# Optimization experiments

Measured on AMD Instinct MI355X. Metric: run time of the kernel, lower is better.

Reference implementation:

```python
import jax, jax.numpy as jnp
import numpy as np

B, L, H = 4, 96, 512
R, T = 257, 21


def setup_inputs() -> dict:
    key = jax.random.key(0)
    ks = jax.random.split(key, 7)
    std_in = (2.0 / (H + 1 + R)) ** 0.5  # xavier_normal over [H+1, R]
    return {
        "layer1": jax.random.normal(ks[0], (B, L, H), jnp.float32),
        "layer2": jax.random.normal(ks[1], (B, L, H), jnp.float32),
        "layer3": jax.random.normal(ks[2], (B, L, H), jnp.float32),
        "W_1": jax.random.normal(ks[3], (H + 1, R), jnp.float32) * std_in,
        "W_2": jax.random.normal(ks[4], (H + 1, R), jnp.float32) * std_in,
        "W_3": jax.random.normal(ks[5], (H + 1, R), jnp.float32) * std_in,
        "W_l": jax.random.normal(ks[6], (1, R, T), jnp.float32),
    }


def reference(layer1, layer2, layer3, W_1, W_2, W_3, W_l):
    # Append bias-ones feature, as in the torch forward.
    ones = jnp.ones((*layer1.shape[:2], 1), layer1.dtype)
    l1 = jnp.concatenate([layer1, ones], axis=-1)  # [n, i, H+1]
    l2 = jnp.concatenate([layer2, ones], axis=-1)  # [n, j, H+1]
    l3 = jnp.concatenate([layer3, jnp.ones((*layer3.shape[:-1], 1), layer3.dtype)], axis=-1)
    # Factor the CP contraction: project each stream to rank space first.
    p1 = jnp.einsum("nia,ar->nir", l1, W_1)  # [n, i, r]
    p2 = jnp.einsum("njb,br->njr", l2, W_2)  # [n, j, r]
    p3 = jnp.einsum("nkc,cr->nkr", l3, W_3)  # [n, k, r]
    # Fold label map into one stream, then rank-reduce outer product.
    p3t = jnp.einsum("nkr,rt->ntkr", p3, W_l[0])  # [n, t, k, r]
    out = jnp.einsum("nir,njr,ntkr->ntijk", p1, p2, p3t)  # [n, t, i, j, k]
    return out
```

## Files before the change

### kernel.cpp

```cpp
#include <hip/hip_runtime.h>
#include <hip/hip_bf16.h>

#define RR 257
#define RP 288
#define TT 21

typedef __attribute__((ext_vector_type(4))) float f32x4;
typedef __attribute__((ext_vector_type(8))) short bf16x8;

union Pack8 { unsigned short s[8]; uint4 v; };

__device__ __forceinline__ unsigned short f2b(float f) {
    union { float f; unsigned u; } v; v.f = f;
    unsigned r = v.u + 0x7fffu + ((v.u >> 16) & 1u);
    return (unsigned short)(r >> 16);
}

__global__ __launch_bounds__(384) void proj_kernel(
    const float* __restrict__ l1, const float* __restrict__ l2, const float* __restrict__ l3,
    const float* __restrict__ W1, const float* __restrict__ W2, const float* __restrict__ W3,
    float* __restrict__ P1f, float* __restrict__ P2f, float* __restrict__ P3f)
{
    int bx = blockIdx.x;
    int grp = bx % 24;
    int n = (bx / 24) & 3;
    int s = bx / 96;
    const float* layer = (s == 0) ? l1 : (s == 1) ? l2 : l3;
    const float* W     = (s == 0) ? W1 : (s == 1) ? W2 : W3;
    int i0 = grp * 4;

    __shared__ __attribute__((aligned(16))) float x[2048];
    const float4* src = (const float4*)(layer + (n * 96 + i0) * 512);
    float4* xv = (float4*)x;
    for (int idx = threadIdx.x; idx < 512; idx += 384) xv[idx] = src[idx];
    __syncthreads();

    int r = threadIdx.x;
    if (r < RP) {
        float a0 = 0.f, a1 = 0.f, a2 = 0.f, a3 = 0.f;
        if (r < RR) {
            float b = W[512 * RR + r];
            a0 = a1 = a2 = a3 = b;
            #pragma unroll 8
            for (int a = 0; a < 512; ++a) {
                float wa = W[a * RR + r];
                a0 = fmaf(x[a], wa, a0);
                a1 = fmaf(x[512 + a], wa, a1);
                a2 = fmaf(x[1024 + a], wa, a2);
                a3 = fmaf(x[1536 + a], wa, a3);
            }
        }
        float* P = (s == 0) ? P1f : (s == 1) ? P2f : P3f;
        int base = (n * 96 + i0) * RP + r;
        P[base]          = a0;
        P[base + RP]     = a1;
        P[base + 2 * RP] = a2;
        P[base + 3 * RP] = a3;
    }
}

__global__ __launch_bounds__(256) void aprep_kernel(
    const float* __restrict__ P1f, const float* __restrict__ P2f,
    unsigned short* __restrict__ Af)
{
    int bx = blockIdx.x;
    int n = bx / 96, i = bx % 96;
    __shared__ __attribute__((aligned(16))) float p1row[RP];
    for (int r = threadIdx.x; r < RP; r += 256)
        p1row[r] = P1f[(n * 96 + i) * RP + r];
    __syncthreads();

    unsigned short* dst = Af + (size_t)(n * 576 + i * 6) * 9 * 512;
    for (int idx = threadIdx.x; idx < 3456; idx += 256) {
        int L = idx & 63;
        int rest = idx >> 6;
        int ks = rest % 9, rgl = rest / 9;
        int j = rgl * 16 + (L & 15);
        int k8 = ks * 32 + (L >> 4) * 8;
        const float* p2p = P2f + (n * 96 + j) * RP + k8;
        float4 b0 = *(const float4*)(p2p);
        float4 b1 = *(const float4*)(p2p + 4);
        float4 a0 = *(const float4*)(p1row + k8);
        float4 a1 = *(const float4*)(p1row + k8 + 4);
        Pack8 u;
        u.s[0] = f2b(a0.x * b0.x); u.s[1] = f2b(a0.y * b0.y);
        u.s[2] = f2b(a0.z * b0.z); u.s[3] = f2b(a0.w * b0.w);
        u.s[4] = f2b(a1.x * b1.x); u.s[5] = f2b(a1.y * b1.y);
        u.s[6] = f2b(a1.z * b1.z); u.s[7] = f2b(a1.w * b1.w);
        *(uint4*)(dst + (size_t)(rgl * 9 + ks) * 512 + L * 8) = u.v;
    }
}

__global__ __launch_bounds__(256) void bprep_kernel(
    const float* __restrict__ P3f, const float* __restrict__ Wl,
    unsigned short* __restrict__ Bf)
{
    int bx = blockIdx.x;
    int t = bx % TT, n = bx / TT;
    __shared__ __attribute__((aligned(16))) float wl_lds[RP];
    for (int r = threadIdx.x; r < RP; r += 256)
        wl_lds[r] = (r < RR) ? Wl[r * TT + t] : 0.f;
    __syncthreads();

    unsigned short* dst = Bf + (size_t)(n * TT + t) * 6 * 9 * 512;
    for (int idx = threadIdx.x; idx < 3456; idx += 256) {
        int L = idx & 63;
        int rest = idx >> 6;
        int ks = rest % 9, kg = rest / 9;
        int col = kg * 16 + (L & 15);
        int r8 = ks * 32 + (L >> 4) * 8;
        const float* p3p = P3f + (n * 96 + col) * RP + r8;
        float4 p0 = *(const float4*)(p3p);
        float4 p1 = *(const float4*)(p3p + 4);
        float4 w0 = *(const float4*)(wl_lds + r8);
        float4 w1 = *(const float4*)(wl_lds + r8 + 4);
        Pack8 u;
        u.s[0] = f2b(p0.x * w0.x); u.s[1] = f2b(p0.y * w0.y);
        u.s[2] = f2b(p0.z * w0.z); u.s[3] = f2b(p0.w * w0.w);
        u.s[4] = f2b(p1.x * w1.x); u.s[5] = f2b(p1.y * w1.y);
        u.s[6] = f2b(p1.z * w1.z); u.s[7] = f2b(p1.w * w1.w);
        *(uint4*)(dst + (size_t)(kg * 9 + ks) * 512 + L * 8) = u.v;
    }
}

#define LOADA(s, kss) { _Pragma("unroll") for (int mf = 0; mf < 4; ++mf) \
    fa[s][mf] = *(const bf16x8*)(abase + (mf * 9 + (kss)) * 512); }
#define LOADB(s, kss) { _Pragma("unroll") for (int nf = 0; nf < 6; ++nf) \
    fb[s][nf] = *(const bf16x8*)(bbase + (nf * 9 + (kss)) * 512); }
#define MFMAS(s) { _Pragma("unroll") for (int mf = 0; mf < 4; ++mf) { \
    _Pragma("unroll") for (int nf = 0; nf < 6; ++nf) \
      acc[mf][nf] = __builtin_amdgcn_mfma_f32_16x16x32_bf16(fb[s][nf], fa[s][mf], acc[mf][nf], 0, 0, 0); } }

__global__ __launch_bounds__(256, 2) void tri4_kernel(
    const unsigned short* __restrict__ Af, const unsigned short* __restrict__ Bf,
    float* __restrict__ out)
{
    int orig = blockIdx.x;
    int bx = (orig & 7) * 378 + (orig >> 3);
    int t = bx % TT;
    int mtn = bx / TT;
    int mt = mtn % 36;
    int n = mtn / 36;

    int tid = threadIdx.x, lane = tid & 63, wv = tid >> 6;

    const unsigned short* abase = Af + (size_t)(n * 576 + mt * 16 + wv * 4) * 9 * 512 + lane * 8;
    const unsigned short* bbase = Bf + (size_t)(n * TT + t) * 6 * 9 * 512 + lane * 8;

    f32x4 acc[4][6] = {};
    bf16x8 fa[2][4], fb[2][6];

    LOADA(0, 0); LOADB(0, 0);
    #pragma unroll
    for (int kp = 0; kp < 4; ++kp) {
        LOADA(1, 2 * kp + 1); LOADB(1, 2 * kp + 1);
        MFMAS(0);
        LOADA(0, 2 * kp + 2); LOADB(0, 2 * kp + 2);
        MFMAS(1);
    }
    MFMAS(0);

    __shared__ __attribute__((aligned(16))) float tbuf[4][1600];
    int Llo = lane & 15, Lhi = lane >> 4;
    size_t outbase = ((size_t)(n * TT + t) * 9216 + mt * 256 + wv * 64) * 96;

    #pragma unroll
    for (int mf = 0; mf < 4; ++mf) {
        #pragma unroll
        for (int nf = 0; nf < 6; ++nf)
            *(f32x4*)&tbuf[wv][Llo * 100 + nf * 16 + Lhi * 4] = acc[mf][nf];
        float* gdst = out + outbase + (size_t)mf * 16 * 96;
        #pragma unroll
        for (int q = 0; q < 6; ++q) {
            int fidx = q * 64 + lane;
            int ml = fidx / 24, k4 = fidx % 24;
            f32x4 vv = *(const f32x4*)&tbuf[wv][ml * 100 + k4 * 4];
            __builtin_nontemporal_store(vv, (f32x4*)(gdst + (size_t)fidx * 4));
        }
    }
}

extern "C" void kernel_launch(void* const* d_in, const int* in_sizes, int n_in,
                              void* d_out, int out_size, void* d_ws, size_t ws_size,
                              hipStream_t stream) {
    const float* l1 = (const float*)d_in[0];
    const float* l2 = (const float*)d_in[1];
    const float* l3 = (const float*)d_in[2];
    const float* W1 = (const float*)d_in[3];
    const float* W2 = (const float*)d_in[4];
    const float* W3 = (const float*)d_in[5];
    const float* Wl = (const float*)d_in[6];

    float* P1f = (float*)d_ws;
    float* P2f = P1f + 384 * RP;
    float* P3f = P2f + 384 * RP;
    unsigned short* Af = (unsigned short*)(P3f + 384 * RP);
    unsigned short* Bf = Af + (size_t)4 * 576 * 9 * 512;

    proj_kernel<<<288, 384, 0, stream>>>(l1, l2, l3, W1, W2, W3, P1f, P2f, P3f);
    aprep_kernel<<<384, 256, 0, stream>>>(P1f, P2f, Af);
    bprep_kernel<<<84, 256, 0, stream>>>(P3f, Wl, Bf);
    tri4_kernel<<<3024, 256, 0, stream>>>(Af, Bf, (float*)d_out);
}
```

Before: 116.6 us.

## Split projection finer, fuse A/B prep kernels, use single-wave output blocks with staggered start

The projection kernel now computes two rows per block instead of four, doubling the grid. The A-prep and B-prep kernels are merged into one launch, with B work split in half across block pairs. The main MFMA kernel drops from four waves per block to one wave per block, quadrupling the grid to 12096 blocks. The first 2048 blocks sleep for a small pseudo-random delay to stagger their write traffic. These changes aim to cut launch count and tail effects, at the risk of more scheduling overhead and idle sleep time.

```diff
diff --git a/kernel.cpp b/kernel.cpp
--- a/kernel.cpp
+++ b/kernel.cpp
@@ -22,104 +22,100 @@
     float* __restrict__ P1f, float* __restrict__ P2f, float* __restrict__ P3f)
 {
     int bx = blockIdx.x;
-    int grp = bx % 24;
-    int n = (bx / 24) & 3;
-    int s = bx / 96;
+    int grp = bx % 48;
+    int n = (bx / 48) & 3;
+    int s = bx / 192;
     const float* layer = (s == 0) ? l1 : (s == 1) ? l2 : l3;
     const float* W     = (s == 0) ? W1 : (s == 1) ? W2 : W3;
-    int i0 = grp * 4;
-
-    __shared__ __attribute__((aligned(16))) float x[2048];
+    int i0 = grp * 2;
+
+    __shared__ __attribute__((aligned(16))) float x[1024];
     const float4* src = (const float4*)(layer + (n * 96 + i0) * 512);
     float4* xv = (float4*)x;
-    for (int idx = threadIdx.x; idx < 512; idx += 384) xv[idx] = src[idx];
+    for (int idx = threadIdx.x; idx < 256; idx += 384) xv[idx] = src[idx];
     __syncthreads();
 
     int r = threadIdx.x;
     if (r < RP) {
-        float a0 = 0.f, a1 = 0.f, a2 = 0.f, a3 = 0.f;
+        float a0 = 0.f, a1 = 0.f;
         if (r < RR) {
             float b = W[512 * RR + r];
-            a0 = a1 = a2 = a3 = b;
+            a0 = a1 = b;
             #pragma unroll 8
             for (int a = 0; a < 512; ++a) {
                 float wa = W[a * RR + r];
                 a0 = fmaf(x[a], wa, a0);
                 a1 = fmaf(x[512 + a], wa, a1);
-                a2 = fmaf(x[1024 + a], wa, a2);
-                a3 = fmaf(x[1536 + a], wa, a3);
             }
         }
         float* P = (s == 0) ? P1f : (s == 1) ? P2f : P3f;
         int base = (n * 96 + i0) * RP + r;
-        P[base]          = a0;
-        P[base + RP]     = a1;
-        P[base + 2 * RP] = a2;
-        P[base + 3 * RP] = a3;
-    }
-}
-
-__global__ __launch_bounds__(256) void aprep_kernel(
+        P[base]      = a0;
+        P[base + RP] = a1;
+    }
+}
+
+__global__ __launch_bounds__(256) void prep_kernel(
     const float* __restrict__ P1f, const float* __restrict__ P2f,
-    unsigned short* __restrict__ Af)
+    const float* __restrict__ P3f, const float* __restrict__ Wl,
+    unsigned short* __restrict__ Af, unsigned short* __restrict__ Bf)
 {
     int bx = blockIdx.x;
-    int n = bx / 96, i = bx % 96;
-    __shared__ __attribute__((aligned(16))) float p1row[RP];
-    for (int r = threadIdx.x; r < RP; r += 256)
-        p1row[r] = P1f[(n * 96 + i) * RP + r];
-    __syncthreads();
-
-    unsigned short* dst = Af + (size_t)(n * 576 + i * 6) * 9 * 512;
-    for (int idx = threadIdx.x; idx < 3456; idx += 256) {
-        int L = idx & 63;
-        int rest = idx >> 6;
-        int ks = rest % 9, rgl = rest / 9;
-        int j = rgl * 16 + (L & 15);
-        int k8 = ks * 32 + (L >> 4) * 8;
-        const float* p2p = P2f + (n * 96 + j) * RP + k8;
-        float4 b0 = *(const float4*)(p2p);
-        float4 b1 = *(const float4*)(p2p + 4);
-        float4 a0 = *(const float4*)(p1row + k8);
-        float4 a1 = *(const float4*)(p1row + k8 + 4);
-        Pack8 u;
-        u.s[0] = f2b(a0.x * b0.x); u.s[1] = f2b(a0.y * b0.y);
-        u.s[2] = f2b(a0.z * b0.z); u.s[3] = f2b(a0.w * b0.w);
-        u.s[4] = f2b(a1.x * b1.x); u.s[5] = f2b(a1.y * b1.y);
-        u.s[6] = f2b(a1.z * b1.z); u.s[7] = f2b(a1.w * b1.w);
-        *(uint4*)(dst + (size_t)(rgl * 9 + ks) * 512 + L * 8) = u.v;
-    }
-}
-
-__global__ __launch_bounds__(256) void bprep_kernel(
-    const float* __restrict__ P3f, const float* __restrict__ Wl,
-    unsigned short* __restrict__ Bf)
-{
-    int bx = blockIdx.x;
-    int t = bx % TT, n = bx / TT;
-    __shared__ __attribute__((aligned(16))) float wl_lds[RP];
-    for (int r = threadIdx.x; r < RP; r += 256)
-        wl_lds[r] = (r < RR) ? Wl[r * TT + t] : 0.f;
-    __syncthreads();
-
-    unsigned short* dst = Bf + (size_t)(n * TT + t) * 6 * 9 * 512;
-    for (int idx = threadIdx.x; idx < 3456; idx += 256) {
-        int L = idx & 63;
-        int rest = idx >> 6;
-        int ks = rest % 9, kg = rest / 9;
-        int col = kg * 16 + (L & 15);
-        int r8 = ks * 32 + (L >> 4) * 8;
-        const float* p3p = P3f + (n * 96 + col) * RP + r8;
-        float4 p0 = *(const float4*)(p3p);
-        float4 p1 = *(const float4*)(p3p + 4);
-        float4 w0 = *(const float4*)(wl_lds + r8);
-        float4 w1 = *(const float4*)(wl_lds + r8 + 4);
-        Pack8 u;
-        u.s[0] = f2b(p0.x * w0.x); u.s[1] = f2b(p0.y * w0.y);
-        u.s[2] = f2b(p0.z * w0.z); u.s[3] = f2b(p0.w * w0.w);
-        u.s[4] = f2b(p1.x * w1.x); u.s[5] = f2b(p1.y * w1.y);
-        u.s[6] = f2b(p1.z * w1.z); u.s[7] = f2b(p1.w * w1.w);
-        *(uint4*)(dst + (size_t)(kg * 9 + ks) * 512 + L * 8) = u.v;
+    if (bx < 384) {
+        int n = bx / 96, i = bx % 96;
+        __shared__ __attribute__((aligned(16))) float p1row[RP];
+        for (int r = threadIdx.x; r < RP; r += 256)
+            p1row[r] = P1f[(n * 96 + i) * RP + r];
+        __syncthreads();
+
+        unsigned short* dst = Af + (size_t)(n * 576 + i * 6) * 9 * 512;
+        for (int idx = threadIdx.x; idx < 3456; idx += 256) {
+            int L = idx & 63;
+            int rest = idx >> 6;
+            int ks = rest % 9, rgl = rest / 9;
+            int j = rgl * 16 + (L & 15);
+            int k8 = ks * 32 + (L >> 4) * 8;
+            const float* p2p = P2f + (n * 96 + j) * RP + k8;
+            float4 b0 = *(const float4*)(p2p);
+            float4 b1 = *(const float4*)(p2p + 4);
+            float4 a0 = *(const float4*)(p1row + k8);
+            float4 a1 = *(const float4*)(p1row + k8 + 4);
+            Pack8 u;
+            u.s[0] = f2b(a0.x * b0.x); u.s[1] = f2b(a0.y * b0.y);
+            u.s[2] = f2b(a0.z * b0.z); u.s[3] = f2b(a0.w * b0.w);
+            u.s[4] = f2b(a1.x * b1.x); u.s[5] = f2b(a1.y * b1.y);
+            u.s[6] = f2b(a1.z * b1.z); u.s[7] = f2b(a1.w * b1.w);
+            *(uint4*)(dst + (size_t)(rgl * 9 + ks) * 512 + L * 8) = u.v;
+        }
+    } else {
+        int b2 = bx - 384;
+        int h = b2 & 1;
+        int t = (b2 >> 1) % TT, n = b2 / (2 * TT);
+        __shared__ __attribute__((aligned(16))) float wl_lds[RP];
+        for (int r = threadIdx.x; r < RP; r += 256)
+            wl_lds[r] = (r < RR) ? Wl[r * TT + t] : 0.f;
+        __syncthreads();
+
+        unsigned short* dst = Bf + (size_t)(n * TT + t) * 6 * 9 * 512;
+        for (int idx2 = threadIdx.x; idx2 < 1728; idx2 += 256) {
+            int idx = h * 1728 + idx2;
+            int L = idx & 63;
+            int rest = idx >> 6;
+            int ks = rest % 9, kg = rest / 9;
+            int col = kg * 16 + (L & 15);
+            int r8 = ks * 32 + (L >> 4) * 8;
+            const float* p3p = P3f + (n * 96 + col) * RP + r8;
+            float4 p0 = *(const float4*)(p3p);
+            float4 p1 = *(const float4*)(p3p + 4);
+            float4 w0 = *(const float4*)(wl_lds + r8);
+            float4 w1 = *(const float4*)(wl_lds + r8 + 4);
+            Pack8 u;
+            u.s[0] = f2b(p0.x * w0.x); u.s[1] = f2b(p0.y * w0.y);
+            u.s[2] = f2b(p0.z * w0.z); u.s[3] = f2b(p0.w * w0.w);
+            u.s[4] = f2b(p1.x * w1.x); u.s[5] = f2b(p1.y * w1.y);
+            u.s[6] = f2b(p1.z * w1.z); u.s[7] = f2b(p1.w * w1.w);
+            *(uint4*)(dst + (size_t)(kg * 9 + ks) * 512 + L * 8) = u.v;
+        }
     }
 }
 
@@ -131,21 +127,27 @@
     _Pragma("unroll") for (int nf = 0; nf < 6; ++nf) \
       acc[mf][nf] = __builtin_amdgcn_mfma_f32_16x16x32_bf16(fb[s][nf], fa[s][mf], acc[mf][nf], 0, 0, 0); } }
 
-__global__ __launch_bounds__(256, 2) void tri4_kernel(
+__global__ __launch_bounds__(64, 2) void tri12_kernel(
     const unsigned short* __restrict__ Af, const unsigned short* __restrict__ Bf,
     float* __restrict__ out)
 {
     int orig = blockIdx.x;
-    int bx = (orig & 7) * 378 + (orig >> 3);
+    if (orig < 2048) {
+        int key = ((orig >> 3) ^ (orig >> 8)) & 7;
+        for (int d = 0; d < key; ++d) __builtin_amdgcn_s_sleep(16);
+    }
+    int bx = (orig & 7) * 1512 + (orig >> 3);
     int t = bx % TT;
     int mtn = bx / TT;
-    int mt = mtn % 36;
-    int n = mtn / 36;
-
-    int tid = threadIdx.x, lane = tid & 63, wv = tid >> 6;
-
-    const unsigned short* abase = Af + (size_t)(n * 576 + mt * 16 + wv * 4) * 9 * 512 + lane * 8;
-    const unsigned short* bbase = Bf + (size_t)(n * TT + t) * 6 * 9 * 512 + lane * 8;
+    int mt = mtn % 144;
+    int n = mtn / 144;
+
+    int lane = threadIdx.x & 63;
+
+    const unsigned short* abase =
+        Af + (size_t)(n * 576 + mt * 4) * 9 * 512 + lane * 8;
+    const unsigned short* bbase =
+        Bf + (size_t)(n * TT + t) * 27648 + lane * 8;
 
     f32x4 acc[4][6] = {};
     bf16x8 fa[2][4], fb[2][6];
@@ -160,21 +162,21 @@
     }
     MFMAS(0);
 
-    __shared__ __attribute__((aligned(16))) float tbuf[4][1600];
+    __shared__ __attribute__((aligned(16))) float tb[1600];
     int Llo = lane & 15, Lhi = lane >> 4;
-    size_t outbase = ((size_t)(n * TT + t) * 9216 + mt * 256 + wv * 64) * 96;
+    size_t outbase = ((size_t)(n * TT + t) * 9216 + mt * 64) * 96;
 
     #pragma unroll
     for (int mf = 0; mf < 4; ++mf) {
         #pragma unroll
         for (int nf = 0; nf < 6; ++nf)
-            *(f32x4*)&tbuf[wv][Llo * 100 + nf * 16 + Lhi * 4] = acc[mf][nf];
+            *(f32x4*)&tb[Llo * 100 + nf * 16 + Lhi * 4] = acc[mf][nf];
         float* gdst = out + outbase + (size_t)mf * 16 * 96;
         #pragma unroll
         for (int q = 0; q < 6; ++q) {
             int fidx = q * 64 + lane;
             int ml = fidx / 24, k4 = fidx % 24;
-            f32x4 vv = *(const f32x4*)&tbuf[wv][ml * 100 + k4 * 4];
+            f32x4 vv = *(const f32x4*)&tb[ml * 100 + k4 * 4];
             __builtin_nontemporal_store(vv, (f32x4*)(gdst + (size_t)fidx * 4));
         }
     }
@@ -197,8 +199,7 @@
     unsigned short* Af = (unsigned short*)(P3f + 384 * RP);
     unsigned short* Bf = Af + (size_t)4 * 576 * 9 * 512;
 
-    proj_kernel<<<288, 384, 0, stream>>>(l1, l2, l3, W1, W2, W3, P1f, P2f, P3f);
-    aprep_kernel<<<384, 256, 0, stream>>>(P1f, P2f, Af);
-    bprep_kernel<<<84, 256, 0, stream>>>(P3f, Wl, Bf);
-    tri4_kernel<<<3024, 256, 0, stream>>>(Af, Bf, (float*)d_out);
-}
+    proj_kernel<<<576, 384, 0, stream>>>(l1, l2, l3, W1, W2, W3, P1f, P2f, P3f);
+    prep_kernel<<<552, 256, 0, stream>>>(P1f, P2f, P3f, Wl, Af, Bf);
+    tri12_kernel<<<12096, 64, 0, stream>>>(Af, Bf, (float*)d_out);
+}
```

Result: faster. 112.2 us (-3.8%).
